# Performance work log

Hardware: AMD Instinct MI355X
Metric: run time of the kernel (lower is better)

The kernel has to match this reference:

```python
import jax, jax.numpy as jnp
import numpy as np

D_MODEL = 1024
N_HEADS = 16
D_K = D_MODEL // N_HEADS
D_FF = 4096
EPS = 1e-5


def _layernorm(x, g, b):
    mu = jnp.mean(x, axis=-1, keepdims=True)
    var = jnp.var(x, axis=-1, keepdims=True)
    return (x - mu) * jax.lax.rsqrt(var + EPS) * g + b


def setup_inputs() -> dict:
    key = jax.random.key(0)
    ks = jax.random.split(key, 12)
    s = 0.02
    x = jax.random.normal(ks[0], (2, 2048, D_MODEL), dtype=jnp.float32)
    # Linear weights stored [in, out] so y = x @ W + b
    wq = jax.random.normal(ks[1], (D_MODEL, D_MODEL), dtype=jnp.float32) * s
    wk = jax.random.normal(ks[2], (D_MODEL, D_MODEL), dtype=jnp.float32) * s
    wv = jax.random.normal(ks[3], (D_MODEL, D_MODEL), dtype=jnp.float32) * s
    wo = jax.random.normal(ks[4], (D_MODEL, D_MODEL), dtype=jnp.float32) * s
    bq = jnp.zeros((D_MODEL,), jnp.float32)
    bk = jnp.zeros((D_MODEL,), jnp.float32)
    bv = jnp.zeros((D_MODEL,), jnp.float32)
    bo = jnp.zeros((D_MODEL,), jnp.float32)
    ln1_g = jnp.ones((D_MODEL,), jnp.float32)
    ln1_b = jnp.zeros((D_MODEL,), jnp.float32)
    ln2_g = jnp.ones((D_MODEL,), jnp.float32)
    ln2_b = jnp.zeros((D_MODEL,), jnp.float32)
    w1 = jax.random.normal(ks[5], (D_MODEL, D_FF), dtype=jnp.float32) * s
    b1 = jnp.zeros((D_FF,), jnp.float32)
    w2 = jax.random.normal(ks[6], (D_FF, D_MODEL), dtype=jnp.float32) * s
    b2 = jnp.zeros((D_MODEL,), jnp.float32)
    return {"x": x, "wq": wq, "bq": bq, "wk": wk, "bk": bk, "wv": wv, "bv": bv,
            "wo": wo, "bo": bo, "ln1_g": ln1_g, "ln1_b": ln1_b,
            "ln2_g": ln2_g, "ln2_b": ln2_b, "w1": w1, "b1": b1, "w2": w2, "b2": b2}


def reference(x, wq, bq, wk, bk, wv, bv, wo, bo, ln1_g, ln1_b, ln2_g, ln2_b, w1, b1, w2, b2):
    B, S, _ = x.shape
    res = x
    # project and split heads: [B, S, H, Dk]
    q = (x @ wq + bq).reshape(B, S, N_HEADS, D_K)
    k = (x @ wk + bk).reshape(B, S, N_HEADS, D_K)
    v = (x @ wv + bv).reshape(B, S, N_HEADS, D_K)
    # full score matrix [B, H, Sq, Sk] (faithful to unfused original)
    scores = jnp.einsum('bqhd,bkhd->bhqk', q, k) / jnp.sqrt(jnp.float32(D_K))
    weights = jax.nn.softmax(scores, axis=-1)
    attn = jnp.einsum('bhqk,bkhd->bqhd', weights, v).reshape(B, S, D_MODEL)
    x = _layernorm(res + attn @ wo + bo, ln1_g, ln1_b)
    res = x
    h = jax.nn.relu(x @ w1 + b1)
    x = _layernorm(res + h @ w2 + b2, ln2_g, ln2_b)
    return x
```

## Files before the change

### kernel.cpp

```cpp
#include <hip/hip_runtime.h>
#include <hip/hip_bf16.h>
#include <stdint.h>


typedef __hip_bfloat16 bf16;
typedef short bf16x8 __attribute__((ext_vector_type(8)));
typedef float f32x4 __attribute__((ext_vector_type(4)));

#if __has_builtin(__builtin_amdgcn_exp2f)
#define EXP2F(x) __builtin_amdgcn_exp2f(x)
#else
#define EXP2F(x) exp2f(x)
#endif

__device__ __forceinline__ float bf2f_lo(unsigned u) { return __uint_as_float(u << 16); }
__device__ __forceinline__ float bf2f_hi(unsigned u) { return __uint_as_float(u & 0xffff0000u); }
__device__ __forceinline__ ushort f2bf(float f) {
  union { bf16 h; ushort u; } c; c.h = __float2bfloat16(f); return c.u;
}
__device__ __forceinline__ uint pk_bf16(float a, float b) {
  union { __hip_bfloat162 h2; uint u; } c;
  c.h2 = __float22bfloat162_rn(make_float2(a, b));
  return c.u;
}
__device__ __forceinline__ bool is_f32(const uint* probe) { return probe[0] == 0x3F800000u; }
__device__ __forceinline__ float ld_param(const void* p, size_t i, bool f32) {
  return f32 ? ((const float*)p)[i] : __bfloat162float(((const bf16*)p)[i]);
}

__device__ __forceinline__ void barrier_raw() {
  asm volatile("" ::: "memory");
  __builtin_amdgcn_s_barrier();
  asm volatile("" ::: "memory");
}
__device__ __forceinline__ void lgkm0() {
  asm volatile("s_waitcnt lgkmcnt(0)" ::: "memory");
}
__device__ __forceinline__ void glds16(const ushort* g, ushort* l) {
  __builtin_amdgcn_global_load_lds(
      (const __attribute__((address_space(1))) void*)g,
      (__attribute__((address_space(3))) void*)l, 16, 0, 0);
}

#define MFMA16(MH, NH)                                                        \
  do {                                                                        \
    _Pragma("unroll") for (int c_ = 0; c_ < 2; ++c_)                          \
    _Pragma("unroll") for (int fi_ = 0; fi_ < 4; ++fi_)                       \
    _Pragma("unroll") for (int gi_ = 0; gi_ < 2; ++gi_)                       \
      acc[(MH) * 4 + fi_][(NH) * 2 + gi_] =                                   \
          __builtin_amdgcn_mfma_f32_16x16x32_bf16(                            \
              areg[fi_][c_], breg[(NH) * 2 + gi_][c_],                        \
              acc[(MH) * 4 + fi_][(NH) * 2 + gi_], 0, 0, 0);                  \
  } while (0)

__device__ __forceinline__ void gemm256_body(
    const ushort* __restrict__ A, const ushort* __restrict__ BT,
    const void* __restrict__ bias, const void* __restrict__ res,
    void* __restrict__ C, int N_, int K_, int bm, int bn,
    int kb, int ke, int mode, const uint* probe) {
  __shared__ ushort As[2][16384];
  __shared__ ushort Bs[2][16384];

  const int tid = threadIdx.x;
  const int wave = tid >> 6;
  const int lane = tid & 63;
  const int wm = wave >> 2;
  const int wn = wave & 3;
  const int m16 = lane & 15;
  const int quad = lane >> 4;
  const int nt = (ke - kb) >> 6;

  const int srow = lane >> 2;
  const int skc = ((lane & 3) * 8) ^ (((lane >> 5) & 1) << 4);
  const ushort* pA = A + (size_t)(bm * 256 + wave * 16 + srow) * K_ + kb + skc;
  const ushort* pB = BT + (size_t)(bn * 256 + wave * 16 + srow) * K_ + kb + skc;
  const size_t hstep = (size_t)128 * K_;
  ushort* dA = &As[0][0] + wave * 1024;
  ushort* dB = &Bs[0][0] + wave * 1024;

  auto stageA = [&](int b, int half, int t) {
    const ushort* g = pA + (size_t)half * hstep + t * 64;
    ushort* d = dA + b * 16384 + half * 8192;
    glds16(g, d);
    glds16(g + 32, d + 512);
  };
  auto stageB = [&](int b, int half, int t) {
    const ushort* g = pB + (size_t)half * hstep + t * 64;
    ushort* d = dB + b * 16384 + half * 8192;
    glds16(g, d);
    glds16(g + 32, d + 512);
  };

  const int fr_off = m16 * 32 + ((quad * 8) ^ (((m16 >> 3) & 1) << 4));
  const ushort* rA = &As[0][0] + fr_off;
  const ushort* rB = &Bs[0][0] + fr_off;
  auto ldA = [&](int b, int f, int c) {
    return *(const bf16x8*)(rA + b * 16384 +
                            ((f >> 2) * 8 + wm * 4 + (f & 3)) * 1024 + c * 512);
  };
  auto ldB = [&](int b, int g, int c) {
    return *(const bf16x8*)(rB + b * 16384 +
                            ((g >> 1) * 8 + wn * 2 + (g & 1)) * 1024 + c * 512);
  };

  f32x4 acc[8][4];
#pragma unroll
  for (int f = 0; f < 8; ++f)
#pragma unroll
    for (int g = 0; g < 4; ++g) acc[f][g] = (f32x4){0.f, 0.f, 0.f, 0.f};
  bf16x8 areg[4][2], breg[4][2];

  stageA(0, 0, 0); stageB(0, 0, 0); stageA(0, 1, 0); stageB(0, 1, 0);
  if (nt > 1) { stageA(1, 0, 1); stageB(1, 0, 1); }
  asm volatile("s_waitcnt vmcnt(4)" ::: "memory");
  barrier_raw();

  for (int t = 0; t < nt; ++t) {
    const int b = t & 1, bo = b ^ 1;
#pragma unroll
    for (int fi = 0; fi < 4; ++fi) { areg[fi][0] = ldA(b, fi, 0); areg[fi][1] = ldA(b, fi, 1); }
#pragma unroll
    for (int gi = 0; gi < 2; ++gi) { breg[gi][0] = ldB(b, gi, 0); breg[gi][1] = ldB(b, gi, 1); }
    if (t + 1 < nt) stageA(bo, 1, t + 1);
    barrier_raw(); lgkm0();
    __builtin_amdgcn_s_setprio(1); MFMA16(0, 0); __builtin_amdgcn_s_setprio(0);
    barrier_raw();
#pragma unroll
    for (int gi = 2; gi < 4; ++gi) { breg[gi][0] = ldB(b, gi, 0); breg[gi][1] = ldB(b, gi, 1); }
    if (t + 1 < nt) stageB(bo, 1, t + 1);
    barrier_raw(); lgkm0();
    __builtin_amdgcn_s_setprio(1); MFMA16(0, 1); __builtin_amdgcn_s_setprio(0);
    barrier_raw();
#pragma unroll
    for (int fi = 0; fi < 4; ++fi) { areg[fi][0] = ldA(b, fi + 4, 0); areg[fi][1] = ldA(b, fi + 4, 1); }
    if (t + 2 < nt) stageA(b, 0, t + 2);
    barrier_raw(); lgkm0();
    __builtin_amdgcn_s_setprio(1); MFMA16(1, 0); __builtin_amdgcn_s_setprio(0);
    barrier_raw();
    if (t + 2 < nt) stageB(b, 0, t + 2);
    barrier_raw(); lgkm0();
    __builtin_amdgcn_s_setprio(1); MFMA16(1, 1); __builtin_amdgcn_s_setprio(0);
    if (t + 2 < nt) asm volatile("s_waitcnt vmcnt(4)" ::: "memory");
    else            asm volatile("s_waitcnt vmcnt(0)" ::: "memory");
    barrier_raw();
  }

  const bool F32 = is_f32(probe);
#pragma unroll
  for (int g = 0; g < 4; ++g) {
    const int col = bn * 256 + (g >> 1) * 128 + wn * 32 + (g & 1) * 16 + m16;
    const float bv = (mode >= 3) ? 0.f : ld_param(bias, col, F32);
#pragma unroll
    for (int f = 0; f < 8; ++f) {
      const int rowb = bm * 256 + (f >> 2) * 128 + wm * 64 + (f & 3) * 16 + quad * 4;
#pragma unroll
      for (int r = 0; r < 4; ++r) {
        const int row = rowb + r;
        float v = acc[f][g][r] + bv;
        if (mode == 1) v = fmaxf(v, 0.f);
        if (mode == 2) v += __bfloat162float(((const bf16*)res)[(size_t)row * N_ + col]);
        if (mode == 2 || mode == 3) ((float*)C)[(size_t)row * N_ + col] = v;
        else ((bf16*)C)[(size_t)row * N_ + col] = __float2bfloat16(v);
      }
    }
  }
}

__global__ __launch_bounds__(512, 2) void gemm256_qkv(
    const ushort* A, const ushort* BT0, const ushort* BT1, const ushort* BT2,
    const void* b0, const void* b1, const void* b2,
    bf16* C0, bf16* C1, bf16* C2, const uint* probe) {
  const int sel = blockIdx.y >> 2, bn = blockIdx.y & 3;
  const ushort* BT = sel == 0 ? BT0 : (sel == 1 ? BT1 : BT2);
  const void* bb = sel == 0 ? b0 : (sel == 1 ? b1 : b2);
  bf16* C = sel == 0 ? C0 : (sel == 1 ? C1 : C2);
  gemm256_body(A, BT, bb, nullptr, C, 1024, 1024, blockIdx.x, bn, 0, 1024, 0, probe);
}
__global__ __launch_bounds__(512, 2) void gemm256_ffn1(
    const ushort* A, const ushort* BT, const void* bias, bf16* C, const uint* probe) {
  gemm256_body(A, BT, bias, nullptr, C, 4096, 1024,
               blockIdx.x, blockIdx.y, 0, 1024, 1, probe);
}
__global__ __launch_bounds__(512, 2) void gemm256_ffn2_sk4(
    const ushort* A, const ushort* BT,
    bf16* P0, bf16* P1, bf16* P2, bf16* P3, const uint* probe) {
  const int kz = blockIdx.z;
  bf16* C = kz == 0 ? P0 : kz == 1 ? P1 : kz == 2 ? P2 : P3;
  gemm256_body(A, BT, nullptr, nullptr, C, 1024, 4096, blockIdx.x, blockIdx.y,
               kz * 1024, kz * 1024 + 1024, 4, probe);
}

template <bool A_EXT, bool RES_EXT>
__device__ __forceinline__ void gemm_body(
    const void* __restrict__ Av, const ushort* __restrict__ BT,
    const void* __restrict__ bias, const void* __restrict__ res,
    void* __restrict__ C, int N_, int K_, int bm, int bn,
    int kb, int ke, int mode, const uint* probe) {
  __shared__ ushort Asm_[128 * 32];
  __shared__ ushort Bsm_[128 * 32];

  const bool F32 = is_f32(probe);
  const bool AF = A_EXT && F32;

  const int tid = threadIdx.x;
  const int wave = tid >> 6;
  const int lane = tid & 63;
  const int wm = wave & 1, wn = wave >> 1;

  const int r0 = tid >> 2;
  const int c0 = (tid & 3) * 8;
  const int dA0 = r0 * 32 + c0;
  const int dA1 = dA0 + 64 * 32;

  const size_t aRow0 = (size_t)(bm * 128 + r0) * K_;
  const size_t aRow1 = aRow0 + (size_t)64 * K_;
  const ushort* pB0 = BT + (size_t)(bn * 128 + r0) * K_ + c0;
  const ushort* pB1 = pB0 + (size_t)64 * K_;

  auto ld4 = [&](int kk, uint4& A0, uint4& A1, uint4& B0, uint4& B1) {
    if (AF) {
      const float* Af = (const float*)Av;
      const float4 f0 = *(const float4*)(Af + aRow0 + kk + c0);
      const float4 f1 = *(const float4*)(Af + aRow0 + kk + c0 + 4);
      const float4 g0 = *(const float4*)(Af + aRow1 + kk + c0);
      const float4 g1 = *(const float4*)(Af + aRow1 + kk + c0 + 4);
      A0.x = pk_bf16(f0.x, f0.y); A0.y = pk_bf16(f0.z, f0.w);
      A0.z = pk_bf16(f1.x, f1.y); A0.w = pk_bf16(f1.z, f1.w);
      A1.x = pk_bf16(g0.x, g0.y); A1.y = pk_bf16(g0.z, g0.w);
      A1.z = pk_bf16(g1.x, g1.y); A1.w = pk_bf16(g1.z, g1.w);
    } else {
      const ushort* Ab = (const ushort*)Av;
      A0 = *(const uint4*)(Ab + aRow0 + kk + c0);
      A1 = *(const uint4*)(Ab + aRow1 + kk + c0);
    }
    B0 = *(const uint4*)(pB0 + kk);
    B1 = *(const uint4*)(pB1 + kk);
  };

  f32x4 zero = {0.f, 0.f, 0.f, 0.f};
  f32x4 acc[4][4];
#pragma unroll
  for (int i = 0; i < 4; ++i)
#pragma unroll
    for (int j = 0; j < 4; ++j) acc[i][j] = zero;

  const int m16 = lane & 15;
  const int quad = lane >> 4;
  const int koff = quad * 8;

  uint4 a0, a1, b0, b1;
  ld4(kb, a0, a1, b0, b1);

  for (int k0 = kb; k0 < ke; k0 += 32) {
    __syncthreads();
    *(uint4*)&Asm_[dA0] = a0;
    *(uint4*)&Asm_[dA1] = a1;
    *(uint4*)&Bsm_[dA0] = b0;
    *(uint4*)&Bsm_[dA1] = b1;
    __syncthreads();

    if (k0 + 32 < ke) ld4(k0 + 32, a0, a1, b0, b1);

    bf16x8 af[4], bfr[4];
#pragma unroll
    for (int i = 0; i < 4; ++i)
      af[i] = *(const bf16x8*)&Asm_[(wm * 64 + i * 16 + m16) * 32 + koff];
#pragma unroll
    for (int j = 0; j < 4; ++j)
      bfr[j] = *(const bf16x8*)&Bsm_[(wn * 64 + j * 16 + m16) * 32 + koff];
#pragma unroll
    for (int i = 0; i < 4; ++i)
#pragma unroll
      for (int j = 0; j < 4; ++j)
        acc[i][j] = __builtin_amdgcn_mfma_f32_16x16x32_bf16(af[i], bfr[j], acc[i][j], 0, 0, 0);
  }

  const int row0 = bm * 128 + wm * 64;
  const int col0 = bn * 128 + wn * 64;
#pragma unroll
  for (int j = 0; j < 4; ++j) {
    const int col = col0 + j * 16 + m16;
    const float bv = (mode == 3) ? 0.f : ld_param(bias, col, F32);
#pragma unroll
    for (int i = 0; i < 4; ++i) {
#pragma unroll
      for (int r = 0; r < 4; ++r) {
        const int row = row0 + i * 16 + quad * 4 + r;
        float v = acc[i][j][r] + bv;
        if (mode == 1) v = fmaxf(v, 0.f);
        if (mode == 2) v += ld_param(res, (size_t)row * N_ + col, RES_EXT && F32);
        if (mode >= 2) ((float*)C)[(size_t)row * N_ + col] = v;
        else ((bf16*)C)[(size_t)row * N_ + col] = __float2bfloat16(v);
      }
    }
  }
}

__global__ __launch_bounds__(256) void gemm_wo_sk(
    const ushort* A, const ushort* BT, const void* bias, const void* res,
    float* C0, float* C1, const uint* probe) {
  const int kz = blockIdx.z;
  gemm_body<false, true>(A, BT, bias, res, kz ? C1 : C0, 1024, 1024,
                         blockIdx.x, blockIdx.y, kz * 512, kz * 512 + 512,
                         kz ? 3 : 2, probe);
}

__global__ __launch_bounds__(256) void transpose_all(
    const void* W0, const void* W1, const void* W2, const void* W3,
    const void* W4, const void* W5, const void* X6,
    ushort* D0, ushort* D1, ushort* D2, ushort* D3, ushort* D4, ushort* D5,
    ushort* D6, const uint* probe) {
  const int z = blockIdx.z;
  if (z == 6) {
    const bool F32 = is_f32(probe);
    const size_t i =
        ((size_t)(blockIdx.y * 128 + blockIdx.x) * 256 + threadIdx.x) * 4;
    if (F32) {
      const float4 a = *(const float4*)((const float*)X6 + i);
      uint2 o; o.x = pk_bf16(a.x, a.y); o.y = pk_bf16(a.z, a.w);
      *(uint2*)(D6 + i) = o;
    } else {
      *(uint2*)(D6 + i) = *(const uint2*)((const ushort*)X6 + i);
    }
    return;
  }
  if (z < 4 && blockIdx.x >= 32) return;
  int n0, k0, K_, N_;
  const void* W;
  ushort* D;
  if (z < 4) {
    n0 = blockIdx.x * 32; k0 = blockIdx.y * 32; K_ = 1024; N_ = 1024;
    W = z == 0 ? W0 : z == 1 ? W1 : z == 2 ? W2 : W3;
    D = z == 0 ? D0 : z == 1 ? D1 : z == 2 ? D2 : D3;
  } else if (z == 4) {
    n0 = blockIdx.x * 32; k0 = blockIdx.y * 32; K_ = 1024; N_ = 4096; W = W4; D = D4;
  } else {
    n0 = blockIdx.y * 32; k0 = blockIdx.x * 32; K_ = 4096; N_ = 1024; W = W5; D = D5;
  }
  const bool F32 = is_f32(probe);
  __shared__ ushort tile[32][33];
  const int tx = threadIdx.x & 31, ty = threadIdx.x >> 5;
#pragma unroll
  for (int i = 0; i < 32; i += 8) {
    const size_t src = (size_t)(k0 + ty + i) * N_ + n0 + tx;
    tile[ty + i][tx] = F32 ? f2bf(((const float*)W)[src]) : ((const ushort*)W)[src];
  }
  __syncthreads();
#pragma unroll
  for (int i = 0; i < 32; i += 8)
    D[(size_t)(n0 + ty + i) * K_ + k0 + tx] = tile[tx][ty + i];
}

__global__ __launch_bounds__(256) void transpose_v(
    const ushort* __restrict__ Vb, ushort* __restrict__ VTp) {
  __shared__ ushort t64[64][66];
  const int tid = threadIdx.x;
  const int ktb = blockIdx.x;
  const int bh = blockIdx.y;
  const int bb = bh >> 4, h = bh & 15;
  const size_t hb = ((size_t)bb * 2048) * 1024 + (size_t)h * 64;
  const int r = tid >> 2, c4 = (tid & 3) * 16;
  const ushort* src = Vb + hb + (size_t)(ktb * 64 + r) * 1024 + c4;
  *(uint4*)&t64[r][c4] = *(const uint4*)src;
  *(uint4*)&t64[r][c4 + 8] = *(const uint4*)(src + 8);
  __syncthreads();
  ushort vals[16];
#pragma unroll
  for (int j = 0; j < 16; ++j) {
    const int jj = c4 + j;
    const int k = 16 * (jj & 3) + (jj >> 2);
    vals[j] = t64[k][r];
  }
  ushort* dst = VTp + (size_t)bh * 131072 + (size_t)r * 2048 + ktb * 64 + c4;
  *(uint4*)dst = *(uint4*)&vals[0];
  *(uint4*)(dst + 8) = *(uint4*)&vals[8];
}

template <bool OUT_EXT>
__global__ __launch_bounds__(256) void ln_kernel(
    const float* __restrict__ X, const float* __restrict__ P,
    const void* __restrict__ g, const void* __restrict__ bta,
    void* __restrict__ out, const uint* probe) {
  const bool F32 = is_f32(probe);
  const int row = blockIdx.x;
  const int tid = threadIdx.x;
  const float4 a = *(const float4*)(X + (size_t)row * 1024 + tid * 4);
  const float4 b = *(const float4*)(P + (size_t)row * 1024 + tid * 4);
  const float xv[4] = {a.x + b.x, a.y + b.y, a.z + b.z, a.w + b.w};
  float s = xv[0] + xv[1] + xv[2] + xv[3];
  float ss = xv[0] * xv[0] + xv[1] * xv[1] + xv[2] * xv[2] + xv[3] * xv[3];
#pragma unroll
  for (int o = 32; o > 0; o >>= 1) { s += __shfl_down(s, o); ss += __shfl_down(ss, o); }
  __shared__ float red[8];
  if ((tid & 63) == 0) { red[tid >> 6] = s; red[4 + (tid >> 6)] = ss; }
  __syncthreads();
  s = red[0] + red[1] + red[2] + red[3];
  ss = red[4] + red[5] + red[6] + red[7];
  const float mu = s * (1.f / 1024.f);
  const float rstd = rsqrtf(ss * (1.f / 1024.f) - mu * mu + 1e-5f);
#pragma unroll
  for (int i = 0; i < 4; ++i) {
    const size_t idx = (size_t)row * 1024 + tid * 4 + i;
    const float y = (xv[i] - mu) * rstd * ld_param(g, tid * 4 + i, F32) +
                    ld_param(bta, tid * 4 + i, F32);
    if (OUT_EXT && F32) ((float*)out)[idx] = y;
    else ((bf16*)out)[idx] = __float2bfloat16(y);
  }
}

template <bool OUT_EXT>
__global__ __launch_bounds__(256) void ln4_kernel(
    const ushort* __restrict__ P0, const ushort* __restrict__ P1,
    const ushort* __restrict__ P2, const ushort* __restrict__ P3,
    const ushort* __restrict__ resX, const void* __restrict__ b2,
    const void* __restrict__ g, const void* __restrict__ bta,
    void* __restrict__ out, const uint* probe) {
  const bool F32 = is_f32(probe);
  const int row = blockIdx.x;
  const int tid = threadIdx.x;
  const size_t base = (size_t)row * 1024 + tid * 4;
  float xv[4];
  {
    const uint2 ur = *(const uint2*)(resX + base);
    xv[0] = bf2f_lo(ur.x) + ld_param(b2, tid * 4 + 0, F32);
    xv[1] = bf2f_hi(ur.x) + ld_param(b2, tid * 4 + 1, F32);
    xv[2] = bf2f_lo(ur.y) + ld_param(b2, tid * 4 + 2, F32);
    xv[3] = bf2f_hi(ur.y) + ld_param(b2, tid * 4 + 3, F32);
  }
  auto addv = [&](const ushort* P) {
    const uint2 u = *(const uint2*)(P + base);
    xv[0] += bf2f_lo(u.x); xv[1] += bf2f_hi(u.x);
    xv[2] += bf2f_lo(u.y); xv[3] += bf2f_hi(u.y);
  };
  addv(P0); addv(P1); addv(P2); addv(P3);
  float s = xv[0] + xv[1] + xv[2] + xv[3];
  float ss = xv[0] * xv[0] + xv[1] * xv[1] + xv[2] * xv[2] + xv[3] * xv[3];
#pragma unroll
  for (int o = 32; o > 0; o >>= 1) { s += __shfl_down(s, o); ss += __shfl_down(ss, o); }
  __shared__ float red[8];
  if ((tid & 63) == 0) { red[tid >> 6] = s; red[4 + (tid >> 6)] = ss; }
  __syncthreads();
  s = red[0] + red[1] + red[2] + red[3];
  ss = red[4] + red[5] + red[6] + red[7];
  const float mu = s * (1.f / 1024.f);
  const float rstd = rsqrtf(ss * (1.f / 1024.f) - mu * mu + 1e-5f);
#pragma unroll
  for (int i = 0; i < 4; ++i) {
    const size_t idx = base + i;
    const float y = (xv[i] - mu) * rstd * ld_param(g, tid * 4 + i, F32) +
                    ld_param(bta, tid * 4 + i, F32);
    if (OUT_EXT && F32) ((float*)out)[idx] = y;
    else ((bf16*)out)[idx] = __float2bfloat16(y);
  }
}

__global__ __launch_bounds__(256, 4) void attn_mfma(
    const ushort* __restrict__ Qm, const ushort* __restrict__ Km,
    const ushort* __restrict__ VTp, ushort* __restrict__ Om) {
  __shared__ ushort Ks[2][4096];
  __shared__ ushort Vs[2][4096];
  __shared__ ushort Pw[4][1024];

  const int tid = threadIdx.x;
  const int wave = tid >> 6, lane = tid & 63;
  const int m16 = lane & 15, quad = lane >> 4;

  const int g = blockIdx.x;
  const int slot = g >> 3;
  const int bh = (g & 7) * 4 + (slot >> 5);
  const int qt = slot & 31;
  const int bb = bh >> 4, h = bh & 15;
  const size_t hb = ((size_t)bb * 2048) * 1024 + (size_t)h * 64;
  const size_t vo = (size_t)bh * 131072;
  const int q0 = qt * 64 + wave * 16;

  const float QS = 0.125f * 1.44269504f;
  const int swz = (m16 >> 3) << 4;
  const int rdo = m16 * 32 + ((quad * 8) ^ swz);

  bf16x8 qf[2];
#pragma unroll
  for (int c = 0; c < 2; ++c) {
    const uint4 u = *(const uint4*)(Qm + hb + (size_t)(q0 + m16) * 1024 + c * 32 + quad * 8);
    const uint w[4] = {u.x, u.y, u.z, u.w};
    bf16x8 f;
#pragma unroll
    for (int j = 0; j < 4; ++j) {
      const uint p = pk_bf16(bf2f_lo(w[j]) * QS, bf2f_hi(w[j]) * QS);
      f[2 * j]     = (short)(p & 0xffffu);
      f[2 * j + 1] = (short)(p >> 16);
    }
    qf[c] = f;
  }

  f32x4 zero = {0.f, 0.f, 0.f, 0.f};
  f32x4 acc[4];
#pragma unroll
  for (int jd = 0; jd < 4; ++jd) acc[jd] = zero;
  float lp[4] = {0.f, 0.f, 0.f, 0.f};

  const int srow = lane >> 2;
  const int skc = ((lane & 3) * 8) ^ ((lane >> 5) << 4);
  const ushort* pK = Km + hb + (size_t)(wave * 16 + srow) * 1024 + skc;
  const ushort* pV = VTp + vo + (size_t)(wave * 16 + srow) * 2048 + skc;
  ushort* dK = &Ks[0][0] + wave * 1024;
  ushort* dV = &Vs[0][0] + wave * 1024;

  glds16(pK, dK);
  glds16(pK + 32, dK + 512);
  glds16(pV, dV);
  glds16(pV + 32, dV + 512);
  asm volatile("s_waitcnt vmcnt(0)" ::: "memory");

  for (int kt = 0; kt < 2048; kt += 64) {
    const int b = (kt >> 6) & 1;
    __syncthreads();
    if (kt + 64 < 2048) {
      const ushort* gk = pK + (size_t)(kt + 64) * 1024;
      const ushort* gv = pV + (kt + 64);
      ushort* dk2 = dK + (b ^ 1) * 4096;
      ushort* dv2 = dV + (b ^ 1) * 4096;
      glds16(gk, dk2);
      glds16(gk + 32, dk2 + 512);
      glds16(gv, dv2);
      glds16(gv + 32, dv2 + 512);
    }

    f32x4 s[4];
#pragma unroll
    for (int jn = 0; jn < 4; ++jn) s[jn] = zero;
    __builtin_amdgcn_s_setprio(1);
#pragma unroll
    for (int c = 0; c < 2; ++c) {
      bf16x8 kb4[4];
#pragma unroll
      for (int jn = 0; jn < 4; ++jn)
        kb4[jn] = *(const bf16x8*)&Ks[b][jn * 1024 + c * 512 + rdo];
#pragma unroll
      for (int jn = 0; jn < 4; ++jn)
        s[jn] = __builtin_amdgcn_mfma_f32_16x16x32_bf16(qf[c], kb4[jn], s[jn], 0, 0, 0);
    }
    __builtin_amdgcn_s_setprio(0);

#pragma unroll
    for (int r = 0; r < 4; ++r) {
      const float p0 = EXP2F(s[0][r]);
      const float p1 = EXP2F(s[1][r]);
      const float p2 = EXP2F(s[2][r]);
      const float p3 = EXP2F(s[3][r]);
      lp[r] += (p0 + p1) + (p2 + p3);
      uint2 pk2;
      pk2.x = pk_bf16(p0, p1);
      pk2.y = pk_bf16(p2, p3);
      const int row = quad * 4 + r;
      *(uint2*)&Pw[wave][(m16 >> 3) * 512 + row * 32 +
                         (((m16 & 7) * 4) ^ ((row >> 3) << 4))] = pk2;
    }
    lgkm0();

    __builtin_amdgcn_s_setprio(1);
#pragma unroll
    for (int c = 0; c < 2; ++c) {
      bf16x8 vb4[4];
      const bf16x8 pa = *(const bf16x8*)&Pw[wave][c * 512 + rdo];
#pragma unroll
      for (int jd = 0; jd < 4; ++jd)
        vb4[jd] = *(const bf16x8*)&Vs[b][jd * 1024 + c * 512 + rdo];
#pragma unroll
      for (int jd = 0; jd < 4; ++jd)
        acc[jd] = __builtin_amdgcn_mfma_f32_16x16x32_bf16(pa, vb4[jd], acc[jd], 0, 0, 0);
    }
    __builtin_amdgcn_s_setprio(0);
    asm volatile("s_waitcnt vmcnt(0)" ::: "memory");
  }

#pragma unroll
  for (int r = 0; r < 4; ++r) {
    float l = lp[r];
    l += __shfl_xor(l, 1); l += __shfl_xor(l, 2);
    l += __shfl_xor(l, 4); l += __shfl_xor(l, 8);
    const float inv = 1.f / l;
    const size_t rowoff = hb + (size_t)(q0 + quad * 4 + r) * 1024;
#pragma unroll
    for (int jd = 0; jd < 4; ++jd)
      Om[rowoff + jd * 16 + m16] = f2bf(acc[jd][r] * inv);
  }
}

extern "C" void kernel_launch(void* const* d_in, const int* in_sizes, int n_in,
                              void* d_out, int out_size, void* d_ws, size_t ws_size,
                              hipStream_t stream) {
  const void* x   = d_in[0];
  const void* wq  = d_in[1];
  const void* bq  = d_in[2];
  const void* wk  = d_in[3];
  const void* bk  = d_in[4];
  const void* wv  = d_in[5];
  const void* bv  = d_in[6];
  const void* wo  = d_in[7];
  const void* bo  = d_in[8];
  const uint* probe = (const uint*)d_in[9];
  const void* ln1g = d_in[9];
  const void* ln1b = d_in[10];
  const void* ln2g = d_in[11];
  const void* ln2b = d_in[12];
  const void* w1  = d_in[13];
  const void* b1  = d_in[14];
  const void* w2  = d_in[15];
  const void* b2  = d_in[16];

  char* ws = (char*)d_ws;
  const size_t MB = 1ull << 20;
  ushort* wqT = (ushort*)(ws + 0 * MB);
  ushort* wkT = (ushort*)(ws + 2 * MB);
  ushort* wvT = (ushort*)(ws + 4 * MB);
  ushort* woT = (ushort*)(ws + 6 * MB);
  ushort* w1T = (ushort*)(ws + 8 * MB);
  ushort* w2T = (ushort*)(ws + 16 * MB);
  ushort* Qb  = (ushort*)(ws + 24 * MB);
  ushort* Kb  = (ushort*)(ws + 32 * MB);
  ushort* Vb  = (ushort*)(ws + 40 * MB);
  ushort* VTp = (ushort*)(ws + 48 * MB);
  ushort* Xb  = (ushort*)(ws + 64 * MB);
  ushort* AO  = (ushort*)(ws + 72 * MB);
  float*  T1  = (float*)(ws + 24 * MB);
  float*  P1w = (float*)(ws + 40 * MB);
  ushort* X1  = (ushort*)(ws + 56 * MB);
  ushort* Hb  = (ushort*)(ws + 24 * MB);
  ushort* P2a = (ushort*)(ws + 0 * MB);
  ushort* P2b = (ushort*)(ws + 8 * MB);
  ushort* P2c = (ushort*)(ws + 64 * MB);
  ushort* P2d = (ushort*)(ws + 72 * MB);

  const dim3 blk(256);
  const dim3 blk512(512);
  transpose_all<<<dim3(128, 32, 7), blk, 0, stream>>>(
      wq, wk, wv, wo, w1, w2, x, wqT, wkT, wvT, woT, w1T, w2T, Xb, probe);

  gemm256_qkv<<<dim3(16, 12), blk512, 0, stream>>>(
      Xb, wqT, wkT, wvT, bq, bk, bv, (bf16*)Qb, (bf16*)Kb, (bf16*)Vb, probe);
  transpose_v<<<dim3(32, 32), blk, 0, stream>>>(Vb, VTp);
  attn_mfma<<<dim3(1024), blk, 0, stream>>>(Qb, Kb, VTp, AO);
  gemm_wo_sk<<<dim3(32, 8, 2), blk, 0, stream>>>(AO, woT, bo, x, T1, P1w, probe);
  ln_kernel<false><<<dim3(4096), blk, 0, stream>>>(T1, P1w, ln1g, ln1b, X1, probe);
  gemm256_ffn1<<<dim3(16, 16), blk512, 0, stream>>>(X1, w1T, b1, (bf16*)Hb, probe);
  gemm256_ffn2_sk4<<<dim3(16, 4, 4), blk512, 0, stream>>>(
      Hb, w2T, (bf16*)P2a, (bf16*)P2b, (bf16*)P2c, (bf16*)P2d, probe);
  ln4_kernel<true><<<dim3(4096), blk, 0, stream>>>(
      P2a, P2b, P2c, P2d, X1, b2, ln2g, ln2b, d_out, probe);
}
```

Measured before the change: 360.2 us.

## Keep softmax probabilities in registers by computing transposed scores in attention

The QK^T MFMA operands are swapped so each lane holds scores for one query across keys. The exponentiated probabilities can then be packed directly into the A-operand fragment for the PV MFMA, with no round trip through the per-wave LDS buffer. The V transpose kernel permutes its key ordering to match the new fragment layout, and the row-sum reduction moves to cross-quad shuffles. A separate lgkmcnt wait is also inserted before a barrier in the GEMM loop. Correctness depends on the key permutation in the V transpose lining up exactly with the register packing order.

```diff
diff --git a/kernel.cpp b/kernel.cpp
--- a/kernel.cpp
+++ b/kernel.cpp
@@ -122,6 +122,7 @@
 #pragma unroll
     for (int gi = 0; gi < 2; ++gi) { breg[gi][0] = ldB(b, gi, 0); breg[gi][1] = ldB(b, gi, 1); }
     if (t + 1 < nt) stageA(bo, 1, t + 1);
+    asm volatile("s_waitcnt lgkmcnt(8)" ::: "memory");
     barrier_raw(); lgkm0();
     __builtin_amdgcn_s_setprio(1); MFMA16(0, 0); __builtin_amdgcn_s_setprio(0);
     barrier_raw();
@@ -368,7 +369,7 @@
 #pragma unroll
   for (int j = 0; j < 16; ++j) {
     const int jj = c4 + j;
-    const int k = 16 * (jj & 3) + (jj >> 2);
+    const int k = 16 * (jj & 3) + 4 * ((jj >> 3) & 3) + 2 * (jj >> 5) + ((jj & 7) >> 2);
     vals[j] = t64[k][r];
   }
   ushort* dst = VTp + (size_t)bh * 131072 + (size_t)r * 2048 + ktb * 64 + c4;
@@ -459,7 +460,6 @@
     const ushort* __restrict__ VTp, ushort* __restrict__ Om) {
   __shared__ ushort Ks[2][4096];
   __shared__ ushort Vs[2][4096];
-  __shared__ ushort Pw[4][1024];
 
   const int tid = threadIdx.x;
   const int wave = tid >> 6, lane = tid & 63;
@@ -497,7 +497,7 @@
   f32x4 acc[4];
 #pragma unroll
   for (int jd = 0; jd < 4; ++jd) acc[jd] = zero;
-  float lp[4] = {0.f, 0.f, 0.f, 0.f};
+  float lp = 0.f;
 
   const int srow = lane >> 2;
   const int skc = ((lane & 3) * 8) ^ ((lane >> 5) << 4);
@@ -538,48 +538,49 @@
         kb4[jn] = *(const bf16x8*)&Ks[b][jn * 1024 + c * 512 + rdo];
 #pragma unroll
       for (int jn = 0; jn < 4; ++jn)
-        s[jn] = __builtin_amdgcn_mfma_f32_16x16x32_bf16(qf[c], kb4[jn], s[jn], 0, 0, 0);
+        s[jn] = __builtin_amdgcn_mfma_f32_16x16x32_bf16(kb4[jn], qf[c], s[jn], 0, 0, 0);
     }
     __builtin_amdgcn_s_setprio(0);
 
-#pragma unroll
-    for (int r = 0; r < 4; ++r) {
-      const float p0 = EXP2F(s[0][r]);
-      const float p1 = EXP2F(s[1][r]);
-      const float p2 = EXP2F(s[2][r]);
-      const float p3 = EXP2F(s[3][r]);
-      lp[r] += (p0 + p1) + (p2 + p3);
-      uint2 pk2;
-      pk2.x = pk_bf16(p0, p1);
-      pk2.y = pk_bf16(p2, p3);
-      const int row = quad * 4 + r;
-      *(uint2*)&Pw[wave][(m16 >> 3) * 512 + row * 32 +
-                         (((m16 & 7) * 4) ^ ((row >> 3) << 4))] = pk2;
-    }
-    lgkm0();
+    float pr[4][4];
+#pragma unroll
+    for (int jn = 0; jn < 4; ++jn) {
+#pragma unroll
+      for (int r = 0; r < 4; ++r) pr[jn][r] = EXP2F(s[jn][r]);
+      lp += (pr[jn][0] + pr[jn][1]) + (pr[jn][2] + pr[jn][3]);
+    }
+    bf16x8 paf[2];
+#pragma unroll
+    for (int c = 0; c < 2; ++c) {
+      union { uint4 u4; bf16x8 v; } cvt;
+      cvt.u4.x = pk_bf16(pr[0][2 * c], pr[1][2 * c]);
+      cvt.u4.y = pk_bf16(pr[2][2 * c], pr[3][2 * c]);
+      cvt.u4.z = pk_bf16(pr[0][2 * c + 1], pr[1][2 * c + 1]);
+      cvt.u4.w = pk_bf16(pr[2][2 * c + 1], pr[3][2 * c + 1]);
+      paf[c] = cvt.v;
+    }
 
     __builtin_amdgcn_s_setprio(1);
 #pragma unroll
     for (int c = 0; c < 2; ++c) {
       bf16x8 vb4[4];
-      const bf16x8 pa = *(const bf16x8*)&Pw[wave][c * 512 + rdo];
 #pragma unroll
       for (int jd = 0; jd < 4; ++jd)
         vb4[jd] = *(const bf16x8*)&Vs[b][jd * 1024 + c * 512 + rdo];
 #pragma unroll
       for (int jd = 0; jd < 4; ++jd)
-        acc[jd] = __builtin_amdgcn_mfma_f32_16x16x32_bf16(pa, vb4[jd], acc[jd], 0, 0, 0);
+        acc[jd] = __builtin_amdgcn_mfma_f32_16x16x32_bf16(paf[c], vb4[jd], acc[jd], 0, 0, 0);
     }
     __builtin_amdgcn_s_setprio(0);
     asm volatile("s_waitcnt vmcnt(0)" ::: "memory");
   }
 
+  float l = lp;
+  l += __shfl_xor(l, 16);
+  l += __shfl_xor(l, 32);
 #pragma unroll
   for (int r = 0; r < 4; ++r) {
-    float l = lp[r];
-    l += __shfl_xor(l, 1); l += __shfl_xor(l, 2);
-    l += __shfl_xor(l, 4); l += __shfl_xor(l, 8);
-    const float inv = 1.f / l;
+    const float inv = 1.f / __shfl(l, quad * 4 + r);
     const size_t rowoff = hb + (size_t)(q0 + quad * 4 + r) * 1024;
 #pragma unroll
     for (int jd = 0; jd < 4; ++jd)
```

After: 361.0 us. About the same (+0.2%).
